# Kernel optimization log

Hardware: AMD Instinct MI355X
Metric: run time of the kernel (lower is better)

Reference implementation:

```python
import jax, jax.numpy as jnp
import numpy as np

B, T, S, E = 16, 1024, 1024, 1024  # note: module requires T == E (see bmm shape constraint)


def setup_inputs() -> dict:
    key = jax.random.key(0)
    ks = jax.random.split(key, 11)
    w = lambda k: jax.random.normal(k, (E, E), dtype=jnp.float32) * 0.02
    b = lambda k: jax.random.normal(k, (E,), dtype=jnp.float32) * 0.02
    return {
        "query": jax.random.normal(ks[0], (B, T, E), dtype=jnp.float32),
        "key": jax.random.normal(ks[1], (B, S, E), dtype=jnp.float32),
        "value": jax.random.normal(ks[2], (B, S, E), dtype=jnp.float32),
        "Wq": w(ks[3]), "bq": b(ks[4]),
        "Wk": w(ks[5]), "bk": b(ks[6]),
        "Wv": w(ks[7]), "bv": b(ks[8]),
        "Wo": w(ks[9]), "bo": b(ks[10]),
    }


def reference(query, key, value, Wq, bq, Wk, bk, Wv, bv, Wo, bo):
    # torch Linear: y = x @ W.T + b
    q = query @ Wq.T + bq          # [B, T, E]
    k = key @ Wk.T + bk            # [B, S, E]
    v = value @ Wv.T + bv          # [B, S, E]
    # Faithful to source: BOTH q and k are transposed to [B, E, len] before bmm,
    # so weights[b, i, s] = sum_t q[b, t, i] * k[b, s, t]  (requires T == E).
    scale = 1.0 / jnp.sqrt(jnp.asarray(q.shape[-1], q.dtype))
    w = jnp.einsum('bti,bst->bis', q, k) * scale   # [B, E, S]
    a = jax.nn.softmax(w, axis=-1)                 # softmax over src_len
    o = jnp.einsum('bis,bse->bie', a, v)           # [B, E, E]
    return o @ Wo.T + bo
```

## Files before the change

kernel.cpp:

```cpp
#include <hip/hip_runtime.h>
#include <hip/hip_bf16.h>
#include <stdint.h>

typedef __attribute__((ext_vector_type(8))) short short8;
typedef __attribute__((ext_vector_type(4))) float floatx4;

#define MODE_PROJ_T 0
#define MODE_PROJ_N 1
#define MODE_SCORES 2
#define MODE_ATT    3
#define MODE_OUT    4

__device__ __forceinline__ unsigned short f2bf(float f) {
    union { float f; unsigned int u; } x; x.f = f;
    unsigned int u = x.u + 0x7FFFu + ((x.u >> 16) & 1u);
    return (unsigned short)(u >> 16);
}

__device__ __forceinline__ void gload_lds16(const void* g, void* lds) {
    __builtin_amdgcn_global_load_lds(
        (const __attribute__((address_space(1))) unsigned int*)g,
        (__attribute__((address_space(3))) unsigned int*)lds,
        16, 0, 0);
}


#define SCHED_PIN() __builtin_amdgcn_sched_barrier(0)

__device__ __forceinline__ void stage_half_A(
    const __hip_bfloat16* __restrict__ Ab, short* lds,
    int row0, int k0, int h, int wid, int lane)
{
    const int rl = lane >> 3, sl = lane & 7;
    const int gcol = k0 + ((sl ^ rl) << 3);
#pragma unroll
    for (int j = 0; j < 2; j++) {
        const int c = wid * 2 + j;
        const int lrow = ((c >> 3) << 7) + h * 64 + ((c & 7) << 3);
        gload_lds16(Ab + (size_t)(row0 + lrow + rl) * 1024 + gcol, lds + lrow * 64);
    }
}

__device__ __forceinline__ void stage_half_B(
    const __hip_bfloat16* __restrict__ Bb, short* lds,
    int col0, int k0, int h, int wid, int lane)
{
    const int rl = lane >> 3, sl = lane & 7;
    const int gcol = k0 + ((sl ^ rl) << 3);
#pragma unroll
    for (int j = 0; j < 2; j++) {
        const int c = wid * 2 + j;
        const int lrow = ((c >> 2) << 6) + h * 32 + ((c & 3) << 3);
        gload_lds16(Bb + (size_t)(col0 + lrow + rl) * 1024 + gcol, lds + lrow * 64);
    }
}

template<int MODE>
__device__ __forceinline__ void gemm_body8(
    const __hip_bfloat16* __restrict__ A,
    const __hip_bfloat16* __restrict__ Bm,
    const float* __restrict__ bias,
    void* __restrict__ Cout,
    int K, long sA, long sB, long sC, float alpha,
    int row0, int col0, int bz, short* As0, short* Bs0)
{
    const int tid  = threadIdx.x;
    const int wid  = tid >> 6;
    const int lane = tid & 63;
    const int wm = wid >> 2, wn = wid & 3;
    const int l15 = lane & 15, quad = lane >> 4, l7 = lane & 7;

    const __hip_bfloat16* Ab = A  + (size_t)bz * sA;
    const __hip_bfloat16* Bb = Bm + (size_t)bz * sB;
    const int NT = K >> 6;

    floatx4 acc[8][4];
#pragma unroll
    for (int i = 0; i < 8; i++)
#pragma unroll
        for (int j = 0; j < 4; j++) acc[i][j] = (floatx4){0.f, 0.f, 0.f, 0.f};

    stage_half_B(Bb, Bs0, col0, 0, 0, wid, lane);
    stage_half_A(Ab, As0, row0, 0, 0, wid, lane);
    stage_half_B(Bb, Bs0, col0, 0, 1, wid, lane);
    stage_half_A(Ab, As0, row0, 0, 1, wid, lane);
    asm volatile("s_waitcnt vmcnt(4)" ::: "memory");
    stage_half_A(Ab, As0 + 16384, row0, 64, 0, wid, lane);
    stage_half_B(Bb, Bs0 + 16384, col0, 64, 1, wid, lane);
    stage_half_A(Ab, As0 + 16384, row0, 64, 1, wid, lane);
    asm volatile("s_waitcnt vmcnt(6)" ::: "memory");
    __builtin_amdgcn_s_barrier();

    for (int t = 0; t < NT; ++t) {
        const int d = t & 1;
        short* Asd = As0 + d * 16384;
        short* Bsd = Bs0 + d * 16384;
        short* Bsn = Bs0 + (d ^ 1) * 16384;
        const int k1 = (t + 1) << 6, k2 = (t + 2) << 6;
        short8 af[4][2], bfr[4][2];

        if (t + 1 < NT) stage_half_B(Bb, Bsn, col0, k1, 0, wid, lane);
#pragma unroll
        for (int mt = 0; mt < 4; mt++)
#pragma unroll
            for (int ks = 0; ks < 2; ks++)
                af[mt][ks] = *(const short8*)&Asd[(wm * 128 + mt * 16 + l15) * 64 +
                                                  ((((ks << 2) + quad) ^ l7) << 3)];
#pragma unroll
        for (int nt = 0; nt < 2; nt++)
#pragma unroll
            for (int ks = 0; ks < 2; ks++)
                bfr[nt][ks] = *(const short8*)&Bsd[(wn * 64 + nt * 16 + l15) * 64 +
                                                   ((((ks << 2) + quad) ^ l7) << 3)];
        asm volatile("s_waitcnt lgkmcnt(8)" ::: "memory");
        SCHED_PIN();
        __builtin_amdgcn_s_barrier();
        asm volatile("s_waitcnt lgkmcnt(0)" ::: "memory");
        SCHED_PIN();
        __builtin_amdgcn_s_setprio(1);
#pragma unroll
        for (int ks = 0; ks < 2; ks++)
#pragma unroll
            for (int mt = 0; mt < 4; mt++)
#pragma unroll
                for (int nt = 0; nt < 2; nt++)
                    acc[mt][nt] = __builtin_amdgcn_mfma_f32_16x16x32_bf16(
                        af[mt][ks], bfr[nt][ks], acc[mt][nt], 0, 0, 0);
        __builtin_amdgcn_s_setprio(0);
        SCHED_PIN();
        __builtin_amdgcn_s_barrier();

        if (t + 2 < NT) stage_half_A(Ab, Asd, row0, k2, 0, wid, lane);
#pragma unroll
        for (int nt = 0; nt < 2; nt++)
#pragma unroll
            for (int ks = 0; ks < 2; ks++)
                bfr[2 + nt][ks] = *(const short8*)&Bsd[(wn * 64 + (2 + nt) * 16 + l15) * 64 +
                                                       ((((ks << 2) + quad) ^ l7) << 3)];
        SCHED_PIN();
        __builtin_amdgcn_s_barrier();
        asm volatile("s_waitcnt lgkmcnt(0)" ::: "memory");
        SCHED_PIN();
        __builtin_amdgcn_s_setprio(1);
#pragma unroll
        for (int ks = 0; ks < 2; ks++)
#pragma unroll
            for (int mt = 0; mt < 4; mt++)
#pragma unroll
                for (int nt = 0; nt < 2; nt++)
                    acc[mt][2 + nt] = __builtin_amdgcn_mfma_f32_16x16x32_bf16(
                        af[mt][ks], bfr[2 + nt][ks], acc[mt][2 + nt], 0, 0, 0);
        __builtin_amdgcn_s_setprio(0);
        SCHED_PIN();
        __builtin_amdgcn_s_barrier();

        if (t + 2 < NT) stage_half_B(Bb, Bsd, col0, k2, 1, wid, lane);
#pragma unroll
        for (int mt = 0; mt < 4; mt++)
#pragma unroll
            for (int ks = 0; ks < 2; ks++)
                af[mt][ks] = *(const short8*)&Asd[(wm * 128 + (4 + mt) * 16 + l15) * 64 +
                                                  ((((ks << 2) + quad) ^ l7) << 3)];
        SCHED_PIN();
        __builtin_amdgcn_s_barrier();
        asm volatile("s_waitcnt lgkmcnt(0)" ::: "memory");
        SCHED_PIN();
        __builtin_amdgcn_s_setprio(1);
#pragma unroll
        for (int ks = 0; ks < 2; ks++)
#pragma unroll
            for (int mt = 0; mt < 4; mt++)
#pragma unroll
                for (int nt = 0; nt < 2; nt++)
                    acc[4 + mt][2 + nt] = __builtin_amdgcn_mfma_f32_16x16x32_bf16(
                        af[mt][ks], bfr[2 + nt][ks], acc[4 + mt][2 + nt], 0, 0, 0);
        __builtin_amdgcn_s_setprio(0);
        SCHED_PIN();
        __builtin_amdgcn_s_barrier();

        if (t + 2 < NT) stage_half_A(Ab, Asd, row0, k2, 1, wid, lane);
        SCHED_PIN();
        __builtin_amdgcn_s_barrier();
        __builtin_amdgcn_s_setprio(1);
#pragma unroll
        for (int ks = 0; ks < 2; ks++)
#pragma unroll
            for (int mt = 0; mt < 4; mt++)
#pragma unroll
                for (int nt = 0; nt < 2; nt++)
                    acc[4 + mt][nt] = __builtin_amdgcn_mfma_f32_16x16x32_bf16(
                        af[mt][ks], bfr[nt][ks], acc[4 + mt][nt], 0, 0, 0);
        __builtin_amdgcn_s_setprio(0);
        SCHED_PIN();
        if (t + 2 < NT) asm volatile("s_waitcnt vmcnt(6)" ::: "memory");
        else            asm volatile("s_waitcnt vmcnt(0)" ::: "memory");
        __builtin_amdgcn_s_barrier();
    }

#pragma unroll
    for (int nt = 0; nt < 4; nt++) {
        const int col = col0 + wn * 64 + nt * 16 + l15;
        float bv = 0.f;
        if (MODE == MODE_PROJ_T || MODE == MODE_PROJ_N || MODE == MODE_OUT) bv = bias[col];
#pragma unroll
        for (int mt = 0; mt < 8; mt++) {
            const int rbase = row0 + wm * 128 + mt * 16 + quad * 4;
            if (MODE == MODE_PROJ_T) {
                ushort4 o;
                o.x = f2bf(acc[mt][nt][0] + bv); o.y = f2bf(acc[mt][nt][1] + bv);
                o.z = f2bf(acc[mt][nt][2] + bv); o.w = f2bf(acc[mt][nt][3] + bv);
                *(ushort4*)&((unsigned short*)Cout)[((size_t)(rbase >> 10) << 20) +
                                                    (size_t)col * 1024 + (rbase & 1023)] = o;
            } else {
#pragma unroll
                for (int r = 0; r < 4; r++) {
                    const int m = rbase + r;
                    float v = acc[mt][nt][r];
                    if (MODE == MODE_SCORES) v *= alpha;
                    v += bv;
                    if (MODE == MODE_SCORES) {
                        ((float*)Cout)[(size_t)bz * sC + (size_t)m * 1024 + col] = v;
                    } else if (MODE == MODE_OUT) {
                        ((float*)Cout)[(size_t)m * 1024 + col] = v;
                    } else {
                        ((unsigned short*)Cout)[(size_t)bz * sC + (size_t)m * 1024 + col] = f2bf(v);
                    }
                }
            }
        }
    }
}

template<int MODE>
__global__ __launch_bounds__(512, 2) void gemm8(
    const __hip_bfloat16* __restrict__ A,
    const __hip_bfloat16* __restrict__ Bm,
    const float* __restrict__ bias,
    void* __restrict__ Cout,
    int K, long sA, long sB, long sC, float alpha)
{
    __shared__ __align__(16) short As[2 * 256 * 64];
    __shared__ __align__(16) short Bs[2 * 256 * 64];
    const int id = blockIdx.x;
    const int xcd = id & 7;
    const int s   = id >> 3;
    int by, bx, bz;
    if (MODE == MODE_SCORES || MODE == MODE_ATT) {
        bz = xcd + ((s >> 4) << 3);
        by = (s & 15) >> 2;
        bx = s & 3;
    } else {
        bz = 0;
        by = ((s >> 2) << 3) | xcd;
        bx = s & 3;
    }
    gemm_body8<MODE>(A, Bm, bias, Cout, K, sA, sB, sC, alpha,
                     by * 256, bx * 256, bz, As, Bs);
}

__global__ __launch_bounds__(512, 2) void gemm8_proj3(
    const __hip_bfloat16* __restrict__ qb, const __hip_bfloat16* __restrict__ kb,
    const __hip_bfloat16* __restrict__ vb,
    const __hip_bfloat16* __restrict__ wq, const __hip_bfloat16* __restrict__ wk,
    const __hip_bfloat16* __restrict__ wv,
    const float* __restrict__ biq, const float* __restrict__ bik,
    const float* __restrict__ biv,
    unsigned short* __restrict__ qT, unsigned short* __restrict__ kp,
    unsigned short* __restrict__ vT)
{
    __shared__ __align__(16) short As[2 * 256 * 64];
    __shared__ __align__(16) short Bs[2 * 256 * 64];
    const int id  = blockIdx.x;
    const int xcd = id & 7;
    const int s   = id >> 3;
    const int g   = s >> 5;
    const int s2  = s & 31;
    const int by  = ((s2 >> 2) << 3) | xcd;
    const int bx  = s2 & 3;
    const __hip_bfloat16* A;  const __hip_bfloat16* B;  const float* bias;  void* C;
    if      (g == 0) { A = qb; B = wq; bias = biq; C = qT; }
    else if (g == 1) { A = kb; B = wk; bias = bik; C = kp; }
    else             { A = vb; B = wv; bias = biv; C = vT; }
    if (g == 1) gemm_body8<MODE_PROJ_N>(A, B, bias, C, 1024, 0, 0, 0, 1.f,
                                        by * 256, bx * 256, 0, As, Bs);
    else        gemm_body8<MODE_PROJ_T>(A, B, bias, C, 1024, 0, 0, 0, 1.f,
                                        by * 256, bx * 256, 0, As, Bs);
}

__global__ __launch_bounds__(256) void softmax_rows(
    const float* __restrict__ S, unsigned short* __restrict__ A)
{
    const int row  = blockIdx.x * 4 + (threadIdx.x >> 6);
    const int lane = threadIdx.x & 63;
    const float4* p = (const float4*)(S + (size_t)row * 1024);
    float4 v[4];
    float mx = -3.0e38f;
#pragma unroll
    for (int i = 0; i < 4; i++) {
        v[i] = p[lane + i * 64];
        mx = fmaxf(mx, fmaxf(fmaxf(v[i].x, v[i].y), fmaxf(v[i].z, v[i].w)));
    }
#pragma unroll
    for (int off = 32; off >= 1; off >>= 1) mx = fmaxf(mx, __shfl_xor(mx, off, 64));
    float e[16], sum = 0.f;
#pragma unroll
    for (int i = 0; i < 4; i++) {
        e[i*4+0] = __expf(v[i].x - mx); e[i*4+1] = __expf(v[i].y - mx);
        e[i*4+2] = __expf(v[i].z - mx); e[i*4+3] = __expf(v[i].w - mx);
        sum += e[i*4+0] + e[i*4+1] + e[i*4+2] + e[i*4+3];
    }
#pragma unroll
    for (int off = 32; off >= 1; off >>= 1) sum += __shfl_xor(sum, off, 64);
    const float inv = 1.0f / sum;
    ushort4* out = (ushort4*)(A + (size_t)row * 1024);
#pragma unroll
    for (int i = 0; i < 4; i++) {
        ushort4 o;
        o.x = f2bf(e[i*4+0] * inv); o.y = f2bf(e[i*4+1] * inv);
        o.z = f2bf(e[i*4+2] * inv); o.w = f2bf(e[i*4+3] * inv);
        out[lane + i * 64] = o;
    }
}

__global__ __launch_bounds__(256) void cvt_all(
    const float* __restrict__ q, const float* __restrict__ k, const float* __restrict__ v,
    const float* __restrict__ wq, const float* __restrict__ wk,
    const float* __restrict__ wv, const float* __restrict__ wo,
    unsigned short* __restrict__ qb, unsigned short* __restrict__ kb, unsigned short* __restrict__ vb,
    unsigned short* __restrict__ wqb, unsigned short* __restrict__ wkb,
    unsigned short* __restrict__ wvb, unsigned short* __restrict__ wob)
{
    const int id = blockIdx.x;
    const float* src; unsigned short* dst; int base;
    if      (id < 16384) { src = q;  dst = qb;  base = 0; }
    else if (id < 32768) { src = k;  dst = kb;  base = 16384; }
    else if (id < 49152) { src = v;  dst = vb;  base = 32768; }
    else if (id < 50176) { src = wq; dst = wqb; base = 49152; }
    else if (id < 51200) { src = wk; dst = wkb; base = 50176; }
    else if (id < 52224) { src = wv; dst = wvb; base = 51200; }
    else                 { src = wo; dst = wob; base = 52224; }
    const int i = (id - base) * 256 + threadIdx.x;
    const float4 vv = ((const float4*)src)[i];
    ushort4 o; o.x = f2bf(vv.x); o.y = f2bf(vv.y); o.z = f2bf(vv.z); o.w = f2bf(vv.w);
    ((ushort4*)dst)[i] = o;
}

extern "C" void kernel_launch(void* const* d_in, const int* in_sizes, int n_in,
                              void* d_out, int out_size, void* d_ws, size_t ws_size,
                              hipStream_t stream) {
    const float* query = (const float*)d_in[0];
    const float* key   = (const float*)d_in[1];
    const float* value = (const float*)d_in[2];
    const float* Wq = (const float*)d_in[3];  const float* bq = (const float*)d_in[4];
    const float* Wk = (const float*)d_in[5];  const float* bk = (const float*)d_in[6];
    const float* Wv = (const float*)d_in[7];  const float* bv = (const float*)d_in[8];
    const float* Wo = (const float*)d_in[9];  const float* bo = (const float*)d_in[10];

    char* ws = (char*)d_ws;
    const size_t MB = 1ull << 20;
    unsigned short* qbf = (unsigned short*)(ws + 0   * MB);
    unsigned short* kbf = (unsigned short*)(ws + 32  * MB);
    unsigned short* vbf = (unsigned short*)(ws + 64  * MB);
    unsigned short* wqb = (unsigned short*)(ws + 96  * MB);
    unsigned short* wkb = (unsigned short*)(ws + 98  * MB);
    unsigned short* wvb = (unsigned short*)(ws + 100 * MB);
    unsigned short* wob = (unsigned short*)(ws + 102 * MB);
    unsigned short* qT  = (unsigned short*)(ws + 104 * MB);
    unsigned short* kp  = (unsigned short*)(ws + 136 * MB);
    unsigned short* vT  = (unsigned short*)(ws + 168 * MB);
    float*          sc  = (float*)(ws + 0 * MB);
    unsigned short* att = (unsigned short*)(ws + 64 * MB);
    unsigned short* ob  = (unsigned short*)(ws + 104 * MB);

    const long S1M = 1 << 20;
    dim3 blk(256);
    dim3 blk5(512);

    cvt_all<<<53248, blk, 0, stream>>>(query, key, value, Wq, Wk, Wv, Wo,
                                       qbf, kbf, vbf, wqb, wkb, wvb, wob);

    gemm8_proj3<<<768, blk5, 0, stream>>>(
        (const __hip_bfloat16*)qbf, (const __hip_bfloat16*)kbf, (const __hip_bfloat16*)vbf,
        (const __hip_bfloat16*)wqb, (const __hip_bfloat16*)wkb, (const __hip_bfloat16*)wvb,
        bq, bk, bv, qT, kp, vT);

    gemm8<MODE_SCORES><<<256, blk5, 0, stream>>>(
        (const __hip_bfloat16*)qT, (const __hip_bfloat16*)kp, nullptr, sc, 1024,
        S1M, S1M, S1M, 0.03125f);

    softmax_rows<<<4096, blk, 0, stream>>>(sc, att);

    gemm8<MODE_ATT><<<256, blk5, 0, stream>>>(
        (const __hip_bfloat16*)att, (const __hip_bfloat16*)vT, nullptr, ob, 1024,
        S1M, S1M, S1M, 1.f);

    gemm8<MODE_OUT><<<256, blk5, 0, stream>>>(
        (const __hip_bfloat16*)ob, (const __hip_bfloat16*)wob, bo, d_out, 1024, 0, 0, 0, 1.f);
}
```

Baseline: 547.6 us.

## Issue LDS fragment reads early and drop redundant barriers in GEMM main loop

Moves the LDS fragment reads for each MFMA phase so they are issued right after the previous MFMA block, before the barrier, instead of after it. The first fragments of the next K-tile are prefetched at the end of the current iteration. Two s_barriers per iteration are removed so LDS latency overlaps with barrier waits and global staging. The added risk is LDS read/write hazards, since the fragment reads now rely on the remaining barriers to order them against the async global_load_lds writes into the same buffers.

```diff
diff --git a/kernel.cpp b/kernel.cpp
--- a/kernel.cpp
+++ b/kernel.cpp
@@ -24,8 +24,9 @@
         16, 0, 0);
 }
 
-
 #define SCHED_PIN() __builtin_amdgcn_sched_barrier(0)
+#define LGKM0() asm volatile("s_waitcnt lgkmcnt(0)" ::: "memory")
+
 
 __device__ __forceinline__ void stage_half_A(
     const __hip_bfloat16* __restrict__ Ab, short* lds,
@@ -79,6 +80,41 @@
     for (int i = 0; i < 8; i++)
 #pragma unroll
         for (int j = 0; j < 4; j++) acc[i][j] = (floatx4){0.f, 0.f, 0.f, 0.f};
+
+    short8 af[4][2], bfr[4][2];
+
+    auto read_a03 = [&](const short* As_) {
+#pragma unroll
+        for (int mt = 0; mt < 4; mt++)
+#pragma unroll
+            for (int ks = 0; ks < 2; ks++)
+                af[mt][ks] = *(const short8*)&As_[(wm * 128 + mt * 16 + l15) * 64 +
+                                                  ((((ks << 2) + quad) ^ l7) << 3)];
+    };
+    auto read_a47 = [&](const short* As_) {
+#pragma unroll
+        for (int mt = 0; mt < 4; mt++)
+#pragma unroll
+            for (int ks = 0; ks < 2; ks++)
+                af[mt][ks] = *(const short8*)&As_[(wm * 128 + (4 + mt) * 16 + l15) * 64 +
+                                                  ((((ks << 2) + quad) ^ l7) << 3)];
+    };
+    auto read_b01 = [&](const short* Bs_) {
+#pragma unroll
+        for (int nt = 0; nt < 2; nt++)
+#pragma unroll
+            for (int ks = 0; ks < 2; ks++)
+                bfr[nt][ks] = *(const short8*)&Bs_[(wn * 64 + nt * 16 + l15) * 64 +
+                                                   ((((ks << 2) + quad) ^ l7) << 3)];
+    };
+    auto read_b23 = [&](const short* Bs_) {
+#pragma unroll
+        for (int nt = 0; nt < 2; nt++)
+#pragma unroll
+            for (int ks = 0; ks < 2; ks++)
+                bfr[2 + nt][ks] = *(const short8*)&Bs_[(wn * 64 + (2 + nt) * 16 + l15) * 64 +
+                                                       ((((ks << 2) + quad) ^ l7) << 3)];
+    };
 
     stage_half_B(Bb, Bs0, col0, 0, 0, wid, lane);
     stage_half_A(Ab, As0, row0, 0, 0, wid, lane);
@@ -90,32 +126,19 @@
     stage_half_A(Ab, As0 + 16384, row0, 64, 1, wid, lane);
     asm volatile("s_waitcnt vmcnt(6)" ::: "memory");
     __builtin_amdgcn_s_barrier();
+    read_a03(As0); read_b01(Bs0);
+    SCHED_PIN();
 
     for (int t = 0; t < NT; ++t) {
         const int d = t & 1;
         short* Asd = As0 + d * 16384;
         short* Bsd = Bs0 + d * 16384;
+        short* Asn = As0 + (d ^ 1) * 16384;
         short* Bsn = Bs0 + (d ^ 1) * 16384;
         const int k1 = (t + 1) << 6, k2 = (t + 2) << 6;
-        short8 af[4][2], bfr[4][2];
 
         if (t + 1 < NT) stage_half_B(Bb, Bsn, col0, k1, 0, wid, lane);
-#pragma unroll
-        for (int mt = 0; mt < 4; mt++)
-#pragma unroll
-            for (int ks = 0; ks < 2; ks++)
-                af[mt][ks] = *(const short8*)&Asd[(wm * 128 + mt * 16 + l15) * 64 +
-                                                  ((((ks << 2) + quad) ^ l7) << 3)];
-#pragma unroll
-        for (int nt = 0; nt < 2; nt++)
-#pragma unroll
-            for (int ks = 0; ks < 2; ks++)
-                bfr[nt][ks] = *(const short8*)&Bsd[(wn * 64 + nt * 16 + l15) * 64 +
-                                                   ((((ks << 2) + quad) ^ l7) << 3)];
-        asm volatile("s_waitcnt lgkmcnt(8)" ::: "memory");
-        SCHED_PIN();
-        __builtin_amdgcn_s_barrier();
-        asm volatile("s_waitcnt lgkmcnt(0)" ::: "memory");
+        LGKM0();
         SCHED_PIN();
         __builtin_amdgcn_s_setprio(1);
 #pragma unroll
@@ -127,19 +150,12 @@
                     acc[mt][nt] = __builtin_amdgcn_mfma_f32_16x16x32_bf16(
                         af[mt][ks], bfr[nt][ks], acc[mt][nt], 0, 0, 0);
         __builtin_amdgcn_s_setprio(0);
+        read_b23(Bsd);
         SCHED_PIN();
         __builtin_amdgcn_s_barrier();
 
         if (t + 2 < NT) stage_half_A(Ab, Asd, row0, k2, 0, wid, lane);
-#pragma unroll
-        for (int nt = 0; nt < 2; nt++)
-#pragma unroll
-            for (int ks = 0; ks < 2; ks++)
-                bfr[2 + nt][ks] = *(const short8*)&Bsd[(wn * 64 + (2 + nt) * 16 + l15) * 64 +
-                                                       ((((ks << 2) + quad) ^ l7) << 3)];
-        SCHED_PIN();
-        __builtin_amdgcn_s_barrier();
-        asm volatile("s_waitcnt lgkmcnt(0)" ::: "memory");
+        LGKM0();
         SCHED_PIN();
         __builtin_amdgcn_s_setprio(1);
 #pragma unroll
@@ -151,19 +167,12 @@
                     acc[mt][2 + nt] = __builtin_amdgcn_mfma_f32_16x16x32_bf16(
                         af[mt][ks], bfr[2 + nt][ks], acc[mt][2 + nt], 0, 0, 0);
         __builtin_amdgcn_s_setprio(0);
+        read_a47(Asd);
         SCHED_PIN();
         __builtin_amdgcn_s_barrier();
 
         if (t + 2 < NT) stage_half_B(Bb, Bsd, col0, k2, 1, wid, lane);
-#pragma unroll
-        for (int mt = 0; mt < 4; mt++)
-#pragma unroll
-            for (int ks = 0; ks < 2; ks++)
-                af[mt][ks] = *(const short8*)&Asd[(wm * 128 + (4 + mt) * 16 + l15) * 64 +
-                                                  ((((ks << 2) + quad) ^ l7) << 3)];
-        SCHED_PIN();
-        __builtin_amdgcn_s_barrier();
-        asm volatile("s_waitcnt lgkmcnt(0)" ::: "memory");
+        LGKM0();
         SCHED_PIN();
         __builtin_amdgcn_s_setprio(1);
 #pragma unroll
@@ -179,8 +188,6 @@
         __builtin_amdgcn_s_barrier();
 
         if (t + 2 < NT) stage_half_A(Ab, Asd, row0, k2, 1, wid, lane);
-        SCHED_PIN();
-        __builtin_amdgcn_s_barrier();
         __builtin_amdgcn_s_setprio(1);
 #pragma unroll
         for (int ks = 0; ks < 2; ks++)
@@ -195,6 +202,10 @@
         if (t + 2 < NT) asm volatile("s_waitcnt vmcnt(6)" ::: "memory");
         else            asm volatile("s_waitcnt vmcnt(0)" ::: "memory");
         __builtin_amdgcn_s_barrier();
+        if (t + 1 < NT) {
+            read_a03(Asn); read_b01(Bsn);
+            SCHED_PIN();
+        }
     }
 
 #pragma unroll
```

Measured after the change: 523.0 us. 1.05x faster.
